# Optimization experiments

Hardware: AMD Instinct MI355X
Metric: run time of the kernel (lower is better)

The kernel has to match this reference:

```python
import jax, jax.numpy as jnp
import numpy as np

E, D_IN, D_OUT = 8, 1024, 1024
B, S = 4, 2048

def setup_inputs() -> dict:
    key = jax.random.key(0)
    k_x, k_g, k_gb, k_w = jax.random.split(key, 4)
    x = jax.random.normal(k_x, (B, S, D_IN), dtype=jnp.float32)
    gate_w = jax.random.normal(k_g, (D_IN, E), dtype=jnp.float32) * 0.02
    gate_b = jax.random.normal(k_gb, (E,), dtype=jnp.float32) * 0.02
    expert_w = jax.random.normal(k_w, (E, D_IN, D_OUT), dtype=jnp.float32) * 0.02
    return {"x": x, "gate_w": gate_w, "gate_b": gate_b, "expert_w": expert_w}

def reference(x, gate_w, gate_b, expert_w):
    # gate: softmax over experts
    gate_score = jax.nn.softmax(x @ gate_w + gate_b, axis=-1)        # [B,S,E]
    # all-expert dense GEMM: [B,S,E,out]
    expert_out = jnp.einsum('bsi,eio->bseo', x, expert_w)
    # gate-weighted combine: [B,S,out]
    out = jnp.einsum('bse,bseo->bso', gate_score, expert_out)
    return out
```

## Files before the change

kernel.cpp:

```cpp
#include <hip/hip_runtime.h>
#include <hip/hip_bf16.h>
#include <cstdint>

#define TOKENS 8192
#define DIN 1024
#define DOUT 1024
#define NE 8

typedef __bf16 bf16;
typedef __attribute__((ext_vector_type(8))) __bf16 bf16x8;
typedef __attribute__((ext_vector_type(4))) float floatx4;
typedef __attribute__((ext_vector_type(2))) float floatx2;

__device__ __forceinline__ void async16(const void* gptr, void* lptr) {
  __builtin_amdgcn_global_load_lds(
      (const __attribute__((address_space(1))) void*)gptr,
      (__attribute__((address_space(3))) void*)lptr,
      16, 0, 0);
}

__global__ __launch_bounds__(256) void prep_kernel(
    const float* __restrict__ x, const float* __restrict__ gw,
    const float* __restrict__ gb, float* __restrict__ g,
    bf16* __restrict__ xb, const float* __restrict__ w,
    bf16* __restrict__ wt) {
  __shared__ float tile[64][65];

  if (blockIdx.x < 2048) {
    const int lane = threadIdx.x & 63;
    const int wave = threadIdx.x >> 6;
    const int t = blockIdx.x * 4 + wave;
    const float* xr = x + (size_t)t * DIN;
    bf16* xbr = xb + (size_t)t * DIN;

    float acc[NE];
#pragma unroll
    for (int e = 0; e < NE; ++e) acc[e] = 0.f;

#pragma unroll
    for (int it = 0; it < 8; ++it) {
      const int i = it * 128 + lane * 2;
      const floatx2 xv = *(const floatx2*)(xr + i);
      union { bf16 b[2]; uint32_t u; } cv;
      cv.b[0] = (bf16)xv[0]; cv.b[1] = (bf16)xv[1];
      *(uint32_t*)(xbr + i) = cv.u;
      const floatx4 w00 = *(const floatx4*)(gw + (size_t)i * NE);
      const floatx4 w01 = *(const floatx4*)(gw + (size_t)i * NE + 4);
      const floatx4 w10 = *(const floatx4*)(gw + (size_t)(i + 1) * NE);
      const floatx4 w11 = *(const floatx4*)(gw + (size_t)(i + 1) * NE + 4);
#pragma unroll
      for (int e = 0; e < 4; ++e) {
        acc[e]     += xv[0] * w00[e] + xv[1] * w10[e];
        acc[e + 4] += xv[0] * w01[e] + xv[1] * w11[e];
      }
    }
#pragma unroll
    for (int e = 0; e < NE; ++e) {
#pragma unroll
      for (int off = 32; off > 0; off >>= 1)
        acc[e] += __shfl_xor(acc[e], off, 64);
    }
    float lg[NE];
    float mx = -3.0e38f;
#pragma unroll
    for (int e = 0; e < NE; ++e) { lg[e] = acc[e] + gb[e]; mx = fmaxf(mx, lg[e]); }
    float s = 0.f;
#pragma unroll
    for (int e = 0; e < NE; ++e) { lg[e] = __expf(lg[e] - mx); s += lg[e]; }
    const float inv = 1.f / s;
    if (lane == 0) {
      floatx4 o0, o1;
#pragma unroll
      for (int e = 0; e < 4; ++e) { o0[e] = lg[e] * inv; o1[e] = lg[e + 4] * inv; }
      *(floatx4*)(g + (size_t)t * NE) = o0;
      *(floatx4*)(g + (size_t)t * NE + 4) = o1;
    }
  } else {
    const int b = blockIdx.x - 2048;
    const int e = b >> 8;
    const int i0 = ((b >> 4) & 15) * 64;
    const int o0 = (b & 15) * 64;
    const int tid = threadIdx.x;
    const int c4 = (tid & 15) * 4;
    const int r = tid >> 4;

    const float* src = w + ((size_t)e * DIN + i0) * DOUT + o0;
#pragma unroll
    for (int rr = r; rr < 64; rr += 16) {
      const floatx4 v = *(const floatx4*)(src + (size_t)rr * DOUT + c4);
      tile[rr][c4] = v[0]; tile[rr][c4 + 1] = v[1];
      tile[rr][c4 + 2] = v[2]; tile[rr][c4 + 3] = v[3];
    }
    __syncthreads();
    bf16* dst = wt + ((size_t)e * DOUT + o0) * DIN + i0;
#pragma unroll
    for (int rr = r; rr < 64; rr += 16) {
      union { bf16 b[4]; uint64_t u; } cv;
#pragma unroll
      for (int j = 0; j < 4; ++j) cv.b[j] = (bf16)tile[c4 + j][rr];
      *(uint64_t*)(dst + (size_t)rr * DIN + c4) = cv.u;
    }
  }
}

__global__ __launch_bounds__(256, 2) void moe_gemm(
    const bf16* __restrict__ xb, const bf16* __restrict__ wt,
    const float* __restrict__ g, float* __restrict__ out) {
  __shared__ __align__(16) bf16 As[128 * 128];
  __shared__ __align__(16) bf16 Bs[128 * 128];

  const int tid = threadIdx.x;
  const int bm = blockIdx.x >> 3;
  const int bn = blockIdx.x & 7;
  const int lane = tid & 63;
  const int wave = tid >> 6;
  const int wm = wave >> 1, wn = wave & 1;
  const int lr = lane & 15, lq = lane >> 4;

  const int srow = tid >> 4;
  const int scol = (((tid & 15) ^ (srow & 7)) << 3);

  const bf16* agp = xb + ((size_t)(bm * 128 + srow)) * DIN + scol;
  bf16* const alp = As + tid * 8;
  bf16* const blp = Bs + tid * 8;

  const int kx = lr & 7;

  const floatx4 fzero = {0.f, 0.f, 0.f, 0.f};
  floatx4 accF[4][4];
#pragma unroll
  for (int im = 0; im < 4; ++im)
#pragma unroll
    for (int in = 0; in < 4; ++in) accF[im][in] = fzero;

  const int tok0 = bm * 128 + wm * 64;

  for (int e = 0; e < NE; ++e) {
    const bf16* bgp = wt + ((size_t)e << 20) +
                      ((size_t)(bn * 128 + srow)) * DIN + scol;
    floatx4 accE[4][4];
#pragma unroll
    for (int im = 0; im < 4; ++im)
#pragma unroll
      for (int in = 0; in < 4; ++in) accE[im][in] = fzero;

    for (int k0 = 0; k0 < DIN; k0 += 128) {
      __syncthreads();
#pragma unroll
      for (int j = 0; j < 8; ++j) {
        async16(agp + k0 + (size_t)(16 * j) * DIN, alp + j * 2048);
        async16(bgp + k0 + (size_t)(16 * j) * DIN, blp + j * 2048);
      }
      __syncthreads();

#pragma unroll
      for (int h = 0; h < 4; ++h) {
        const int kg = ((h * 4 + lq) ^ kx) << 3;
        bf16x8 av[4], bv[4];
#pragma unroll
        for (int im = 0; im < 4; ++im)
          av[im] = *(const bf16x8*)(As + (wm * 64 + im * 16 + lr) * 128 + kg);
#pragma unroll
        for (int in = 0; in < 4; ++in)
          bv[in] = *(const bf16x8*)(Bs + (wn * 64 + in * 16 + lr) * 128 + kg);
#pragma unroll
        for (int im = 0; im < 4; ++im)
#pragma unroll
          for (int in = 0; in < 4; ++in)
            accE[im][in] = __builtin_amdgcn_mfma_f32_16x16x32_bf16(
                av[im], bv[in], accE[im][in], 0, 0, 0);
      }
    }

#pragma unroll
    for (int im = 0; im < 4; ++im) {
      float gv[4];
#pragma unroll
      for (int r = 0; r < 4; ++r)
        gv[r] = g[(size_t)(tok0 + im * 16 + lq * 4 + r) * NE + e];
#pragma unroll
      for (int in = 0; in < 4; ++in)
#pragma unroll
        for (int r = 0; r < 4; ++r)
          accF[im][in][r] += gv[r] * accE[im][in][r];
    }
  }

#pragma unroll
  for (int im = 0; im < 4; ++im)
#pragma unroll
    for (int in = 0; in < 4; ++in) {
      const int col = bn * 128 + wn * 64 + in * 16 + lr;
#pragma unroll
      for (int r = 0; r < 4; ++r)
        out[(size_t)(tok0 + im * 16 + lq * 4 + r) * DOUT + col] =
            accF[im][in][r];
    }
}

extern "C" void kernel_launch(void* const* d_in, const int* in_sizes, int n_in,
                              void* d_out, int out_size, void* d_ws,
                              size_t ws_size, hipStream_t stream) {
  const float* x  = (const float*)d_in[0];
  const float* gw = (const float*)d_in[1];
  const float* gb = (const float*)d_in[2];
  const float* w  = (const float*)d_in[3];
  float* out = (float*)d_out;

  char* ws = (char*)d_ws;
  float* g  = (float*)ws;
  bf16* xb  = (bf16*)(ws + 262144);
  bf16* wt  = (bf16*)(ws + 262144 + (size_t)TOKENS * DIN * 2);

  prep_kernel<<<4096, 256, 0, stream>>>(x, gw, gb, g, xb, w, wt);
  moe_gemm<<<512, 256, 0, stream>>>(xb, wt, g, out);
}
```

Measured before the change: 270.1 us.

## Stage gate weights in LDS for gating and remap GEMM blocks for L2 locality

The gating part of the prep kernel now loads the whole gate weight matrix into shared memory, transposed per expert, and each block handles 16 tokens with float4 x loads. Before, every wave re-read the weights from global memory for each token. The GEMM block index is also remapped so blocks that run together share row and column tiles, which should improve L2 reuse across the XCD-style block distribution. In exchange, the 32KB of shared memory per prep block may lower occupancy, and the transposed writes into shared memory may cause bank conflicts.

```diff
diff --git a/kernel.cpp b/kernel.cpp
--- a/kernel.cpp
+++ b/kernel.cpp
@@ -24,59 +24,73 @@
     const float* __restrict__ gb, float* __restrict__ g,
     bf16* __restrict__ xb, const float* __restrict__ w,
     bf16* __restrict__ wt) {
-  __shared__ float tile[64][65];
-
-  if (blockIdx.x < 2048) {
-    const int lane = threadIdx.x & 63;
-    const int wave = threadIdx.x >> 6;
-    const int t = blockIdx.x * 4 + wave;
-    const float* xr = x + (size_t)t * DIN;
-    bf16* xbr = xb + (size_t)t * DIN;
-
-    float acc[NE];
-#pragma unroll
-    for (int e = 0; e < NE; ++e) acc[e] = 0.f;
-
-#pragma unroll
-    for (int it = 0; it < 8; ++it) {
-      const int i = it * 128 + lane * 2;
-      const floatx2 xv = *(const floatx2*)(xr + i);
-      union { bf16 b[2]; uint32_t u; } cv;
-      cv.b[0] = (bf16)xv[0]; cv.b[1] = (bf16)xv[1];
-      *(uint32_t*)(xbr + i) = cv.u;
-      const floatx4 w00 = *(const floatx4*)(gw + (size_t)i * NE);
-      const floatx4 w01 = *(const floatx4*)(gw + (size_t)i * NE + 4);
-      const floatx4 w10 = *(const floatx4*)(gw + (size_t)(i + 1) * NE);
-      const floatx4 w11 = *(const floatx4*)(gw + (size_t)(i + 1) * NE + 4);
-#pragma unroll
-      for (int e = 0; e < 4; ++e) {
-        acc[e]     += xv[0] * w00[e] + xv[1] * w10[e];
-        acc[e + 4] += xv[0] * w01[e] + xv[1] * w11[e];
-      }
-    }
-#pragma unroll
-    for (int e = 0; e < NE; ++e) {
-#pragma unroll
-      for (int off = 32; off > 0; off >>= 1)
-        acc[e] += __shfl_xor(acc[e], off, 64);
-    }
-    float lg[NE];
-    float mx = -3.0e38f;
-#pragma unroll
-    for (int e = 0; e < NE; ++e) { lg[e] = acc[e] + gb[e]; mx = fmaxf(mx, lg[e]); }
-    float s = 0.f;
-#pragma unroll
-    for (int e = 0; e < NE; ++e) { lg[e] = __expf(lg[e] - mx); s += lg[e]; }
-    const float inv = 1.f / s;
-    if (lane == 0) {
-      floatx4 o0, o1;
-#pragma unroll
-      for (int e = 0; e < 4; ++e) { o0[e] = lg[e] * inv; o1[e] = lg[e + 4] * inv; }
-      *(floatx4*)(g + (size_t)t * NE) = o0;
-      *(floatx4*)(g + (size_t)t * NE + 4) = o1;
+  __shared__ __align__(16) float smem[NE * DIN];
+
+  if (blockIdx.x < 512) {
+    const int tid = threadIdx.x;
+#pragma unroll
+    for (int k = 0; k < 8; ++k) {
+      const int base = (k * 256 + tid) * 4;
+      const floatx4 v = *(const floatx4*)(gw + base);
+#pragma unroll
+      for (int m = 0; m < 4; ++m) {
+        const int j = base + m;
+        smem[(j & 7) * DIN + (j >> 3)] = v[m];
+      }
+    }
+    __syncthreads();
+
+    const int lane = tid & 63;
+    const int wave = tid >> 6;
+#pragma unroll
+    for (int tt = 0; tt < 4; ++tt) {
+      const int t = blockIdx.x * 16 + wave * 4 + tt;
+      const float* xr = x + (size_t)t * DIN;
+      bf16* xbr = xb + (size_t)t * DIN;
+
+      float acc[NE];
+#pragma unroll
+      for (int e = 0; e < NE; ++e) acc[e] = 0.f;
+
+#pragma unroll
+      for (int it = 0; it < 4; ++it) {
+        const int i = it * 256 + lane * 4;
+        const floatx4 xv = *(const floatx4*)(xr + i);
+        union { bf16 b[4]; uint64_t u; } cv;
+#pragma unroll
+        for (int m = 0; m < 4; ++m) cv.b[m] = (bf16)xv[m];
+        *(uint64_t*)(xbr + i) = cv.u;
+#pragma unroll
+        for (int e = 0; e < NE; ++e) {
+          const floatx4 wv = *(const floatx4*)(smem + e * DIN + i);
+          acc[e] += xv[0] * wv[0] + xv[1] * wv[1] + xv[2] * wv[2] + xv[3] * wv[3];
+        }
+      }
+#pragma unroll
+      for (int e = 0; e < NE; ++e)
+#pragma unroll
+        for (int off = 32; off > 0; off >>= 1)
+          acc[e] += __shfl_xor(acc[e], off, 64);
+
+      float lg[NE];
+      float mx = -3.0e38f;
+#pragma unroll
+      for (int e = 0; e < NE; ++e) { lg[e] = acc[e] + gb[e]; mx = fmaxf(mx, lg[e]); }
+      float s = 0.f;
+#pragma unroll
+      for (int e = 0; e < NE; ++e) { lg[e] = __expf(lg[e] - mx); s += lg[e]; }
+      const float inv = 1.f / s;
+      if (lane == 0) {
+        floatx4 o0, o1;
+#pragma unroll
+        for (int e = 0; e < 4; ++e) { o0[e] = lg[e] * inv; o1[e] = lg[e + 4] * inv; }
+        *(floatx4*)(g + (size_t)t * NE) = o0;
+        *(floatx4*)(g + (size_t)t * NE + 4) = o1;
+      }
     }
   } else {
-    const int b = blockIdx.x - 2048;
+    float (*tile)[65] = (float(*)[65])smem;
+    const int b = blockIdx.x - 512;
     const int e = b >> 8;
     const int i0 = ((b >> 4) & 15) * 64;
     const int o0 = (b & 15) * 64;
@@ -110,8 +124,10 @@
   __shared__ __align__(16) bf16 Bs[128 * 128];
 
   const int tid = threadIdx.x;
-  const int bm = blockIdx.x >> 3;
-  const int bn = blockIdx.x & 7;
+  const int c = blockIdx.x & 7;
+  const int jj = blockIdx.x >> 3;
+  const int bm = (c >> 1) * 16 + (jj & 15);
+  const int bn = (c & 1) * 4 + (jj >> 4);
   const int lane = tid & 63;
   const int wave = tid >> 6;
   const int wm = wave >> 1, wn = wave & 1;
@@ -212,6 +228,6 @@
   bf16* xb  = (bf16*)(ws + 262144);
   bf16* wt  = (bf16*)(ws + 262144 + (size_t)TOKENS * DIN * 2);
 
-  prep_kernel<<<4096, 256, 0, stream>>>(x, gw, gb, g, xb, w, wt);
+  prep_kernel<<<2560, 256, 0, stream>>>(x, gw, gb, g, xb, w, wt);
   moe_gemm<<<512, 256, 0, stream>>>(xb, wt, g, out);
 }
```

Result: faster. 238.7 us (-11.6%).
